# Kernel optimization log

Hardware: AMD Instinct MI355X
Metric: run time of the kernel (lower is better)

Reference implementation:

```python
import jax, jax.numpy as jnp
import numpy as np

NUM_WORDS = 1024
EMBED_DIM = 1024
NUM_SAMPLES = 65536


def setup_inputs() -> dict:
    key = jax.random.key(0)
    k1, k2, k3, k4 = jax.random.split(key, 4)
    return {
        "word_embeddings": jax.random.normal(k1, (NUM_WORDS, EMBED_DIM), dtype=jnp.float32),
        "t_query": jax.random.uniform(k2, (NUM_SAMPLES,), dtype=jnp.float32),
        "tension_params": jax.random.normal(k3, (NUM_WORDS - 1,), dtype=jnp.float32),
        "semantic_weights": jnp.ones((EMBED_DIM,), dtype=jnp.float32),
        "word_biases": jax.random.normal(k4, (NUM_WORDS, EMBED_DIM), dtype=jnp.float32),
        "curvature_controls": jnp.ones((NUM_WORDS,), dtype=jnp.float32),
    }


def reference(word_embeddings, t_query, tension_params, semantic_weights, word_biases, curvature_controls):
    N, D = word_embeddings.shape
    # adjusted + semantic weighting
    emb = (word_embeddings + word_biases) * semantic_weights[None, :]  # [N, D]

    # t_words = linspace(0, 1, N): segment index = floor(t * (N-1)), clipped to [0, N-2]
    scaled = t_query * (N - 1)
    seg = jnp.clip(jnp.floor(scaled).astype(jnp.int32), 0, N - 2)  # [S]
    t = scaled - seg.astype(t_query.dtype)  # local parameter in [0, 1]

    # control points via batched gather
    p0 = emb[jnp.maximum(seg - 1, 0)]       # [S, D]
    p1 = emb[seg]
    p2 = emb[seg + 1]
    p3 = emb[jnp.minimum(seg + 2, N - 1)]

    tension = jax.nn.sigmoid(tension_params[seg])  # [S]
    c1 = curvature_controls[seg]
    c2 = curvature_controls[seg + 1]

    t2 = t * t
    t3 = t2 * t
    v0 = (-0.5 * t3 + t2 - 0.5 * t) * tension
    v1 = (1.5 * t3 - 2.5 * t2 + 1.0) * c1
    v2 = (-1.5 * t3 + 2.0 * t2 + 0.5 * t) * c2
    v3 = (0.5 * t3 - 0.5 * t2) * tension
    total = v0 + v1 + v2 + v3
    v0, v1, v2, v3 = v0 / total, v1 / total, v2 / total, v3 / total

    out = (v0[:, None] * p0 + v1[:, None] * p1 + v2[:, None] * p2 + v3[:, None] * p3)  # [S, D]

    # boundary handling: t <= 0 -> emb[0], t >= 1 -> emb[-1]
    out = jnp.where((t_query <= 0.0)[:, None], emb[0][None, :], out)
    out = jnp.where((t_query >= 1.0)[:, None], emb[-1][None, :], out)
    return out
```

## Files before the change

kernel.cpp:

```cpp
#include <hip/hip_runtime.h>
#include <hip/hip_bf16.h>
#include <math.h>

#define NW 1024
#define ED 1024
#define NS 65536
#define ED4 (ED / 4)
#define CAP 256
#define CHUNKS 4

#define REC_OFF  0u
#define CUR_OFF  (NW * CAP * 16u)

__global__ __launch_bounds__(256) void scatter_kernel(
    const float* __restrict__ tq, const float* __restrict__ tp,
    const float* __restrict__ cc, int* __restrict__ curs,
    float4* __restrict__ recs)
{
    int s = blockIdx.x * 256 + threadIdx.x;
    float q = tq[s];
    float scaled = q * (float)(NW - 1);
    int seg = (int)floorf(scaled);
    seg = min(max(seg, 0), NW - 2);
    float t = scaled - (float)seg;

    float tension = 1.0f / (1.0f + expf(-tp[seg]));
    float c1 = cc[seg], c2 = cc[seg + 1];
    float t2 = t * t, t3 = t2 * t;
    float v0 = (-0.5f * t3 + t2 - 0.5f * t) * tension;
    float v1 = (1.5f * t3 - 2.5f * t2 + 1.0f) * c1;
    float v2 = (-1.5f * t3 + 2.0f * t2 + 0.5f * t) * c2;
    float v3 = (0.5f * t3 - 0.5f * t2) * tension;
    float inv = 1.0f / (v0 + v1 + v2 + v3);
    v0 *= inv; v1 *= inv; v2 *= inv;

    if (q <= 0.0f) { v0 = 1.0f; v1 = 0.0f; v2 = 0.0f; }
    if (q >= 1.0f) { v0 = 0.0f; v1 = 0.0f; v2 = 1.0f; }

    int pos = atomicAdd(&curs[seg], 1);
    if (pos < CAP) {
        float4 r;
        r.x = v0; r.y = v1; r.z = v2;
        r.w = __int_as_float(s);
        recs[seg * CAP + pos] = r;
    }
}

__global__ __launch_bounds__(256) void out_kernel(
    const float4* __restrict__ we4, const float4* __restrict__ wb4,
    const float4* __restrict__ sw4, const int* __restrict__ curs,
    const float4* __restrict__ recs, float4* __restrict__ out4)
{
    const int seg   = blockIdx.x >> 2;
    const int chunk = blockIdx.x & (CHUNKS - 1);
    const int tid   = threadIdx.x;

    const int n = min(curs[seg], CAP);
    if (chunk >= n) return;

    const int r0 = max(seg - 1, 0);
    const int r3 = min(seg + 2, NW - 1);
    const float4 s = sw4[tid];

    float4 w0 = we4[r0 * ED4 + tid],      b0 = wb4[r0 * ED4 + tid];
    float4 w1 = we4[seg * ED4 + tid],     b1 = wb4[seg * ED4 + tid];
    float4 w2 = we4[(seg+1) * ED4 + tid], b2 = wb4[(seg+1) * ED4 + tid];
    float4 w3 = we4[r3 * ED4 + tid],      b3 = wb4[r3 * ED4 + tid];

    float4 a, b, c, d;
    a.x = (w0.x + b0.x) * s.x; a.y = (w0.y + b0.y) * s.y;
    a.z = (w0.z + b0.z) * s.z; a.w = (w0.w + b0.w) * s.w;
    b.x = (w1.x + b1.x) * s.x; b.y = (w1.y + b1.y) * s.y;
    b.z = (w1.z + b1.z) * s.z; b.w = (w1.w + b1.w) * s.w;
    c.x = (w2.x + b2.x) * s.x; c.y = (w2.y + b2.y) * s.y;
    c.z = (w2.z + b2.z) * s.z; c.w = (w2.w + b2.w) * s.w;
    d.x = (w3.x + b3.x) * s.x; d.y = (w3.y + b3.y) * s.y;
    d.z = (w3.z + b3.z) * s.z; d.w = (w3.w + b3.w) * s.w;

    const float4* __restrict__ rec = recs + seg * CAP;

#define EMIT(wv)                                                        \
    do {                                                                \
        float vw_ = 1.0f - (wv).x - (wv).y - (wv).z;                    \
        int sid_ = __float_as_int((wv).w);                              \
        float4 r_;                                                      \
        r_.x = (wv).x * a.x + (wv).y * b.x + (wv).z * c.x + vw_ * d.x;  \
        r_.y = (wv).x * a.y + (wv).y * b.y + (wv).z * c.y + vw_ * d.y;  \
        r_.z = (wv).x * a.z + (wv).y * b.z + (wv).z * c.z + vw_ * d.z;  \
        r_.w = (wv).x * a.w + (wv).y * b.w + (wv).z * c.w + vw_ * d.w;  \
        out4[(size_t)sid_ * ED4 + tid] = r_;                            \
    } while (0)

    int k = chunk;
    for (; k + 3 * CHUNKS < n; k += 4 * CHUNKS) {
        float4 rA = rec[k];
        float4 rB = rec[k + CHUNKS];
        float4 rC = rec[k + 2 * CHUNKS];
        float4 rD = rec[k + 3 * CHUNKS];
        EMIT(rA);
        EMIT(rB);
        EMIT(rC);
        EMIT(rD);
    }
    for (; k < n; k += CHUNKS) {
        float4 rA = rec[k];
        EMIT(rA);
    }
#undef EMIT
}

extern "C" void kernel_launch(void* const* d_in, const int* in_sizes, int n_in,
                              void* d_out, int out_size, void* d_ws, size_t ws_size,
                              hipStream_t stream) {
    const float* we = (const float*)d_in[0];
    const float* tq = (const float*)d_in[1];
    const float* tp = (const float*)d_in[2];
    const float* sw = (const float*)d_in[3];
    const float* wb = (const float*)d_in[4];
    const float* cc = (const float*)d_in[5];
    float* out = (float*)d_out;

    char* ws = (char*)d_ws;
    float4* recs = (float4*)(ws + REC_OFF);
    int*    curs = (int*)(ws + CUR_OFF);

    hipMemsetAsync(curs, 0, NW * sizeof(int), stream);

    scatter_kernel<<<NS / 256, 256, 0, stream>>>(tq, tp, cc, curs, recs);

    out_kernel<<<NW * CHUNKS, 256, 0, stream>>>(
        (const float4*)we, (const float4*)wb, (const float4*)sw,
        curs, recs, (float4*)out);
}
```

Measured before the change: 295.2 us.

## Precompute weighted embeddings once and halve out-kernel chunks per segment

Adds a pre-pass kernel that computes (embeddings + biases) * weights once into workspace and zeroes the per-segment counters, replacing the memset. The output kernel now reads four precomputed rows instead of eight raw rows plus the weight vector, which removes redundant loads and arithmetic repeated per chunk block. The number of blocks per segment drops from four to two, so each block does more samples and the grid is smaller. This costs an extra launch and an 8 MB read plus 4 MB write pass, and may lower parallelism in the output stage.

After: 298.2 us. About the same (+1.0%).

```diff
diff --git a/kernel.cpp b/kernel.cpp
--- a/kernel.cpp
+++ b/kernel.cpp
@@ -7,10 +7,29 @@
 #define NS 65536
 #define ED4 (ED / 4)
 #define CAP 256
-#define CHUNKS 4
+#define CHUNKS 2
 
-#define REC_OFF  0u
-#define CUR_OFF  (NW * CAP * 16u)
+#define EMB_OFF  0u
+#define REC_OFF  (4u * 1024u * 1024u)
+#define CUR_OFF  (REC_OFF + NW * CAP * 16u)
+
+__global__ __launch_bounds__(256) void emb_precompute_kernel(
+    const float4* __restrict__ we, const float4* __restrict__ wb,
+    const float4* __restrict__ sw, float4* __restrict__ emb,
+    int* __restrict__ curs)
+{
+    int i = blockIdx.x * 256 + threadIdx.x;
+    if (i < NW) curs[i] = 0;
+    float4 w = we[i];
+    float4 b = wb[i];
+    float4 s = sw[i & (ED4 - 1)];
+    float4 r;
+    r.x = (w.x + b.x) * s.x;
+    r.y = (w.y + b.y) * s.y;
+    r.z = (w.z + b.z) * s.z;
+    r.w = (w.w + b.w) * s.w;
+    emb[i] = r;
+}
 
 __global__ __launch_bounds__(256) void scatter_kernel(
     const float* __restrict__ tq, const float* __restrict__ tp,
@@ -47,11 +66,10 @@
 }
 
 __global__ __launch_bounds__(256) void out_kernel(
-    const float4* __restrict__ we4, const float4* __restrict__ wb4,
-    const float4* __restrict__ sw4, const int* __restrict__ curs,
+    const float4* __restrict__ emb4, const int* __restrict__ curs,
     const float4* __restrict__ recs, float4* __restrict__ out4)
 {
-    const int seg   = blockIdx.x >> 2;
+    const int seg   = blockIdx.x >> 1;
     const int chunk = blockIdx.x & (CHUNKS - 1);
     const int tid   = threadIdx.x;
 
@@ -60,22 +78,11 @@
 
     const int r0 = max(seg - 1, 0);
     const int r3 = min(seg + 2, NW - 1);
-    const float4 s = sw4[tid];
 
-    float4 w0 = we4[r0 * ED4 + tid],      b0 = wb4[r0 * ED4 + tid];
-    float4 w1 = we4[seg * ED4 + tid],     b1 = wb4[seg * ED4 + tid];
-    float4 w2 = we4[(seg+1) * ED4 + tid], b2 = wb4[(seg+1) * ED4 + tid];
-    float4 w3 = we4[r3 * ED4 + tid],      b3 = wb4[r3 * ED4 + tid];
-
-    float4 a, b, c, d;
-    a.x = (w0.x + b0.x) * s.x; a.y = (w0.y + b0.y) * s.y;
-    a.z = (w0.z + b0.z) * s.z; a.w = (w0.w + b0.w) * s.w;
-    b.x = (w1.x + b1.x) * s.x; b.y = (w1.y + b1.y) * s.y;
-    b.z = (w1.z + b1.z) * s.z; b.w = (w1.w + b1.w) * s.w;
-    c.x = (w2.x + b2.x) * s.x; c.y = (w2.y + b2.y) * s.y;
-    c.z = (w2.z + b2.z) * s.z; c.w = (w2.w + b2.w) * s.w;
-    d.x = (w3.x + b3.x) * s.x; d.y = (w3.y + b3.y) * s.y;
-    d.z = (w3.z + b3.z) * s.z; d.w = (w3.w + b3.w) * s.w;
+    float4 a = emb4[r0 * ED4 + tid];
+    float4 b = emb4[seg * ED4 + tid];
+    float4 c = emb4[(seg + 1) * ED4 + tid];
+    float4 d = emb4[r3 * ED4 + tid];
 
     const float4* __restrict__ rec = recs + seg * CAP;
 
@@ -121,14 +128,16 @@
     float* out = (float*)d_out;
 
     char* ws = (char*)d_ws;
+    float*  emb  = (float*)(ws + EMB_OFF);
     float4* recs = (float4*)(ws + REC_OFF);
     int*    curs = (int*)(ws + CUR_OFF);
 
-    hipMemsetAsync(curs, 0, NW * sizeof(int), stream);
+    emb_precompute_kernel<<<1024, 256, 0, stream>>>(
+        (const float4*)we, (const float4*)wb, (const float4*)sw,
+        (float4*)emb, curs);
 
     scatter_kernel<<<NS / 256, 256, 0, stream>>>(tq, tp, cc, curs, recs);
 
     out_kernel<<<NW * CHUNKS, 256, 0, stream>>>(
-        (const float4*)we, (const float4*)wb, (const float4*)sw,
-        curs, recs, (float4*)out);
+        (const float4*)emb, curs, recs, (float4*)out);
 }
```
